# Kernel optimization log

Hardware: AMD Instinct MI355X
Metric: run time of the kernel (lower is better)

## Reference

```python
import jax, jax.numpy as jnp
import numpy as np
import math

NUM_HEADS = 8
LN_EPS = 1e-5
SINK_EPS = 1.0  # entropic eps in SinkhornDistance (eps=1)


def _layer_norm(x, g, b):
    m = jnp.mean(x, axis=-1, keepdims=True)
    v = jnp.var(x, axis=-1, keepdims=True)
    return (x - m) * jax.lax.rsqrt(v + LN_EPS) * g + b


def setup_inputs() -> dict:
    key = jax.random.key(0)
    ks = jax.random.split(key, 8)
    B, n, dQ, dV = 8, 1024, 512, 512
    s = 1.0 / math.sqrt(dV)
    return {
        "Q": jax.random.normal(ks[0], (B, n, dQ), jnp.float32),
        "K": jax.random.normal(ks[1], (B, n, dQ), jnp.float32),
        "Wq": jax.random.normal(ks[2], (dV, dQ), jnp.float32) * s,
        "bq": jax.random.normal(ks[3], (dV,), jnp.float32) * 0.01,
        "Wo": jax.random.normal(ks[4], (dV, dV), jnp.float32) * s,
        "bo": jax.random.normal(ks[5], (dV,), jnp.float32) * 0.01,
        "g0": jnp.ones((dV,), jnp.float32),
        "b0": jnp.zeros((dV,), jnp.float32),
        "g1": jnp.ones((dV,), jnp.float32),
        "b1": jnp.zeros((dV,), jnp.float32),
    }


def reference(Q, K, Wq, bq, Wo, bo, g0, b0, g1, b1):
    # K is accepted by the original forward but unused (K_ = V_ = Q_).
    B, n, _ = Q.shape
    dim_V = Wq.shape[0]
    H = NUM_HEADS
    d = dim_V // H

    Qp = Q @ Wq.T + bq                                   # [B, n, dim_V]
    # torch.cat(Q.split(d, 2), 0): head-major stacking -> [H*B, n, d]
    Q_ = Qp.reshape(B, n, H, d).transpose(2, 0, 1, 3).reshape(H * B, n, d)

    sqrtV = math.sqrt(math.sqrt(dim_V))
    X = Q_ / sqrtV
    # cost = dotmat(X, X) = -X X^T  (overall scaled by 1/sqrt(dim_V))
    C = -jnp.einsum('bnd,bmd->bnm', X, X)                # [HB, n, n]

    # log-domain Sinkhorn, eps=1, max_iter=1, mu = nu = 1/n
    log_mu = jnp.log(1.0 / n + 1e-8).astype(Q.dtype)
    M0 = -C / SINK_EPS
    u = SINK_EPS * (log_mu - jax.scipy.special.logsumexp(M0, axis=-1))         # [HB, n]
    v = SINK_EPS * (log_mu - jax.scipy.special.logsumexp(
        (-C + u[:, :, None]) / SINK_EPS, axis=1))                               # [HB, n]
    pi = jnp.exp((-C + u[:, :, None] + v[:, None, :]) / SINK_EPS)               # [HB, n, n]

    A = pi * n
    O_ = Q_ + jnp.einsum('bnm,bmd->bnd', A, Q_)          # [HB, n, d]
    # inverse head stacking -> [B, n, dim_V]
    O = O_.reshape(H, B, n, d).transpose(1, 2, 0, 3).reshape(B, n, dim_V)

    O = _layer_norm(O, g0, b0)
    O = O + jax.nn.relu(O @ Wo.T + bo)
    O = _layer_norm(O, g1, b1)
    return O
```

## Files before the change

kernel.cpp:

```cpp
#include <hip/hip_runtime.h>
#include <hip/hip_bf16.h>

typedef __bf16 bf16;
typedef __bf16 bf16x4 __attribute__((ext_vector_type(4)));
typedef __bf16 bf16x8 __attribute__((ext_vector_type(8)));
typedef float  f32x4  __attribute__((ext_vector_type(4)));

#define DEVI static __device__ __forceinline__

constexpr float SCALE_S = 0.04419417382415922f;
constexpr float LOG_MU  = -6.93146156565f;
constexpr int   LDT     = 72;

DEVI f32x4 mfma16(bf16x8 a, bf16x8 b, f32x4 c) {
    return __builtin_amdgcn_mfma_f32_16x16x32_bf16(a, b, c, 0, 0, 0);
}

DEVI bf16x8 cvt8(const float* __restrict__ p) {
    const float4 f0 = *(const float4*)p;
    const float4 f1 = *(const float4*)(p + 4);
    bf16x8 h;
    h[0] = (bf16)f0.x; h[1] = (bf16)f0.y; h[2] = (bf16)f0.z; h[3] = (bf16)f0.w;
    h[4] = (bf16)f1.x; h[5] = (bf16)f1.y; h[6] = (bf16)f1.z; h[7] = (bf16)f1.w;
    return h;
}

template<int EPI>
__global__ __launch_bounds__(256)
void gemm_kernel(const void* __restrict__ Ap, const float* __restrict__ Bm,
                 const float* __restrict__ bias, const bf16* __restrict__ X0,
                 bf16* __restrict__ outQh, bf16* __restrict__ outQhT,
                 float* __restrict__ outT)
{
    __shared__ bf16 sA[64 * LDT];
    __shared__ bf16 sB[64 * LDT];
    const int tid = threadIdx.x;
    const int rowBase = blockIdx.y * 64;
    const int colBase = blockIdx.x * 64;
    const int w = tid >> 6, lane = tid & 63, quad = lane >> 4, l16 = lane & 15;
    const int wr = (w >> 1) * 32, wc = (w & 1) * 32;

    f32x4 acc[2][2];
    #pragma unroll
    for (int i = 0; i < 2; ++i)
        #pragma unroll
        for (int j = 0; j < 2; ++j)
            #pragma unroll
            for (int e = 0; e < 4; ++e) acc[i][j][e] = 0.f;

    for (int kt = 0; kt < 512; kt += 64) {
        if (kt) __syncthreads();
        #pragma unroll
        for (int it = 0; it < 2; ++it) {
            int idx = it * 256 + tid;
            int r = idx >> 3, kb = idx & 7;
            if (EPI == 0) {
                *(bf16x8*)(&sA[r * LDT + kb * 8]) =
                    cvt8((const float*)Ap + (size_t)(rowBase + r) * 512 + kt + kb * 8);
            } else {
                *(uint4*)(&sA[r * LDT + kb * 8]) =
                    *(const uint4*)((const bf16*)Ap + (size_t)(rowBase + r) * 512 + kt + kb * 8);
            }
            *(bf16x8*)(&sB[r * LDT + kb * 8]) =
                cvt8(Bm + (size_t)(colBase + r) * 512 + kt + kb * 8);
        }
        __syncthreads();
        #pragma unroll
        for (int kk = 0; kk < 2; ++kk) {
            bf16x8 a[2], b[2];
            #pragma unroll
            for (int i = 0; i < 2; ++i)
                a[i] = *(const bf16x8*)(&sA[(wr + i * 16 + l16) * LDT + kk * 32 + quad * 8]);
            #pragma unroll
            for (int j = 0; j < 2; ++j)
                b[j] = *(const bf16x8*)(&sB[(wc + j * 16 + l16) * LDT + kk * 32 + quad * 8]);
            #pragma unroll
            for (int i = 0; i < 2; ++i)
                #pragma unroll
                for (int j = 0; j < 2; ++j)
                    acc[i][j] = mfma16(a[i], b[j], acc[i][j]);
        }
    }

    #pragma unroll
    for (int i = 0; i < 2; ++i) {
        #pragma unroll
        for (int j = 0; j < 2; ++j) {
            const int col = colBase + wc + j * 16 + l16;
            const float bv = bias[col];
            if (EPI == 0) {
                const int hh = col >> 6, jj = col & 63;
                const int rowA = rowBase + wr + i * 16 + quad * 4;
                const int bb = rowA >> 10, iib = rowA & 1023;
                const int bhh = (hh << 3) + bb;
                bf16x4 pk;
                #pragma unroll
                for (int rg = 0; rg < 4; ++rg) {
                    const float z = acc[i][j][rg] + bv;
                    pk[rg] = (bf16)z;
                    outQh[((size_t)(bhh * 1024 + iib + rg) << 6) + jj] = (bf16)z;
                }
                if (outQhT)
                    *(bf16x4*)(&outQhT[(((size_t)bhh * 64 + jj) << 10) + iib]) = pk;
            } else {
                #pragma unroll
                for (int rg = 0; rg < 4; ++rg) {
                    const int row = rowBase + wr + i * 16 + quad * 4 + rg;
                    const float z = acc[i][j][rg] + bv;
                    const float x0 = (float)X0[(size_t)row * 512 + col];
                    outT[(size_t)row * 512 + col] = x0 + fmaxf(z, 0.f);
                }
            }
        }
    }
}

template<int ADD_U>
__global__ __launch_bounds__(256, 4)
void sink_lse_kernel(const bf16* __restrict__ Qh, const float* __restrict__ uin,
                     float* __restrict__ out)
{
    __shared__ bf16 sQi[128 * LDT];
    __shared__ bf16 sQm[64 * LDT];
    __shared__ float su[1024];
    const int tid = threadIdx.x;
    const int bh = blockIdx.y;
    const int rowTile = blockIdx.x * 128;
    const bf16* Qb = Qh + ((size_t)bh << 16);

    #pragma unroll
    for (int it = 0; it < 4; ++it) {
        int idx = it * 256 + tid;
        int r = idx >> 3, kb = idx & 7;
        *(uint4*)(&sQi[r * LDT + kb * 8]) =
            *(const uint4*)(Qb + ((rowTile + r) << 6) + kb * 8);
    }
    if (ADD_U)
        *(float4*)(&su[tid * 4]) = *(const float4*)(uin + (bh << 10) + tid * 4);

    const int w = tid >> 6, lane = tid & 63, quad = lane >> 4, l16 = lane & 15;
    float rsum[2][4] = {{0.f,0.f,0.f,0.f},{0.f,0.f,0.f,0.f}};

    for (int mt = 0; mt < 16; ++mt) {
        __syncthreads();
        #pragma unroll
        for (int it = 0; it < 2; ++it) {
            int idx = it * 256 + tid;
            int r = idx >> 3, kb = idx & 7;
            *(uint4*)(&sQm[r * LDT + kb * 8]) =
                *(const uint4*)(Qb + ((mt * 64 + r) << 6) + kb * 8);
        }
        __syncthreads();

        f32x4 acc[2][4];
        #pragma unroll
        for (int a = 0; a < 2; ++a)
            #pragma unroll
            for (int ct = 0; ct < 4; ++ct)
                #pragma unroll
                for (int e = 0; e < 4; ++e) acc[a][ct][e] = 0.f;

        #pragma unroll
        for (int kk = 0; kk < 2; ++kk) {
            bf16x8 afr[2], bfr[4];
            #pragma unroll
            for (int a = 0; a < 2; ++a)
                afr[a] = *(const bf16x8*)(&sQi[(w * 32 + a * 16 + l16) * LDT + kk * 32 + quad * 8]);
            #pragma unroll
            for (int ct = 0; ct < 4; ++ct)
                bfr[ct] = *(const bf16x8*)(&sQm[(ct * 16 + l16) * LDT + kk * 32 + quad * 8]);
            #pragma unroll
            for (int a = 0; a < 2; ++a)
                #pragma unroll
                for (int ct = 0; ct < 4; ++ct)
                    acc[a][ct] = mfma16(afr[a], bfr[ct], acc[a][ct]);
        }
        #pragma unroll
        for (int a = 0; a < 2; ++a)
            #pragma unroll
            for (int ct = 0; ct < 4; ++ct) {
                const float uadd = ADD_U ? su[mt * 64 + ct * 16 + l16] : 0.f;
                #pragma unroll
                for (int rg = 0; rg < 4; ++rg)
                    rsum[a][rg] += __expf(acc[a][ct][rg] * SCALE_S + uadd);
            }
    }
    #pragma unroll
    for (int off = 1; off < 16; off <<= 1)
        #pragma unroll
        for (int a = 0; a < 2; ++a)
            #pragma unroll
            for (int rg = 0; rg < 4; ++rg)
                rsum[a][rg] += __shfl_xor(rsum[a][rg], off);

    if (l16 == 0) {
        #pragma unroll
        for (int a = 0; a < 2; ++a)
            #pragma unroll
            for (int rg = 0; rg < 4; ++rg)
                out[(bh << 10) + rowTile + w * 32 + a * 16 + quad * 4 + rg] =
                    LOG_MU - __logf(rsum[a][rg]);
    }
}

template<int USE_T>
__global__ __launch_bounds__(256, 2)
void sink_av_kernel(const bf16* __restrict__ Qh, const bf16* __restrict__ QhT,
                    const float* __restrict__ u, const float* __restrict__ v,
                    float* __restrict__ O)
{
    __shared__ bf16 sQi[128 * LDT];
    __shared__ bf16 sQm[64 * LDT];
    __shared__ bf16 sQmT[64 * LDT];
    __shared__ bf16 sP[4][32 * LDT];
    __shared__ float sv[1024];
    const int tid = threadIdx.x;
    const int bh = blockIdx.y;
    const int rowTile = blockIdx.x * 128;
    const bf16* Qb = Qh + ((size_t)bh << 16);
    const bf16* QbT = QhT + ((size_t)bh << 16);
    const int w = tid >> 6, lane = tid & 63, quad = lane >> 4, l16 = lane & 15;

    #pragma unroll
    for (int it = 0; it < 4; ++it) {
        int idx = it * 256 + tid;
        int r = idx >> 3, kb = idx & 7;
        *(uint4*)(&sQi[r * LDT + kb * 8]) =
            *(const uint4*)(Qb + ((rowTile + r) << 6) + kb * 8);
    }
    *(float4*)(&sv[tid * 4]) = *(const float4*)(v + (bh << 10) + tid * 4);
    float u_r[2][4];
    #pragma unroll
    for (int a = 0; a < 2; ++a)
        #pragma unroll
        for (int rg = 0; rg < 4; ++rg)
            u_r[a][rg] = u[(bh << 10) + rowTile + w * 32 + a * 16 + quad * 4 + rg];

    f32x4 accO[2][4];
    #pragma unroll
    for (int a = 0; a < 2; ++a)
        #pragma unroll
        for (int ct = 0; ct < 4; ++ct)
            #pragma unroll
            for (int e = 0; e < 4; ++e) accO[a][ct][e] = 0.f;

    for (int mt = 0; mt < 16; ++mt) {
        __syncthreads();
        #pragma unroll
        for (int it = 0; it < 2; ++it) {
            int idx = it * 256 + tid;
            int r = idx >> 3, kb = idx & 7;
            if (USE_T) {
                *(uint4*)(&sQm[r * LDT + kb * 8]) =
                    *(const uint4*)(Qb + ((mt * 64 + r) << 6) + kb * 8);
                *(uint4*)(&sQmT[r * LDT + kb * 8]) =
                    *(const uint4*)(QbT + (r << 10) + mt * 64 + kb * 8);
            } else {
                uint4 val = *(const uint4*)(Qb + ((mt * 64 + r) << 6) + kb * 8);
                *(uint4*)(&sQm[r * LDT + kb * 8]) = val;
                union { uint4 q; bf16 e[8]; } cv; cv.q = val;
                #pragma unroll
                for (int j = 0; j < 8; ++j)
                    sQmT[(kb * 8 + j) * LDT + r] = cv.e[j];
            }
        }
        __syncthreads();

        f32x4 acc[2][4];
        #pragma unroll
        for (int a = 0; a < 2; ++a)
            #pragma unroll
            for (int ct = 0; ct < 4; ++ct)
                #pragma unroll
                for (int e = 0; e < 4; ++e) acc[a][ct][e] = 0.f;

        #pragma unroll
        for (int kk = 0; kk < 2; ++kk) {
            bf16x8 afr[2], bfr[4];
            #pragma unroll
            for (int a = 0; a < 2; ++a)
                afr[a] = *(const bf16x8*)(&sQi[(w * 32 + a * 16 + l16) * LDT + kk * 32 + quad * 8]);
            #pragma unroll
            for (int ct = 0; ct < 4; ++ct)
                bfr[ct] = *(const bf16x8*)(&sQm[(ct * 16 + l16) * LDT + kk * 32 + quad * 8]);
            #pragma unroll
            for (int a = 0; a < 2; ++a)
                #pragma unroll
                for (int ct = 0; ct < 4; ++ct)
                    acc[a][ct] = mfma16(afr[a], bfr[ct], acc[a][ct]);
        }
        #pragma unroll
        for (int a = 0; a < 2; ++a)
            #pragma unroll
            for (int ct = 0; ct < 4; ++ct) {
                const float vv = sv[mt * 64 + ct * 16 + l16];
                #pragma unroll
                for (int rg = 0; rg < 4; ++rg) {
                    const float p = 1024.f * __expf(acc[a][ct][rg] * SCALE_S + u_r[a][rg] + vv);
                    sP[w][(a * 16 + quad * 4 + rg) * LDT + ct * 16 + l16] = (bf16)p;
                }
            }
        #pragma unroll
        for (int kk = 0; kk < 2; ++kk) {
            bf16x8 a2[2], b2[4];
            #pragma unroll
            for (int a = 0; a < 2; ++a)
                a2[a] = *(const bf16x8*)(&sP[w][(a * 16 + l16) * LDT + kk * 32 + quad * 8]);
            #pragma unroll
            for (int ct = 0; ct < 4; ++ct)
                b2[ct] = *(const bf16x8*)(&sQmT[(ct * 16 + l16) * LDT + kk * 32 + quad * 8]);
            #pragma unroll
            for (int a = 0; a < 2; ++a)
                #pragma unroll
                for (int ct = 0; ct < 4; ++ct)
                    accO[a][ct] = mfma16(a2[a], b2[ct], accO[a][ct]);
        }
    }

    const int hh = bh >> 3, bb = bh & 7;
    #pragma unroll
    for (int a = 0; a < 2; ++a)
        #pragma unroll
        for (int ct = 0; ct < 4; ++ct) {
            const int dcol = ct * 16 + l16;
            #pragma unroll
            for (int rg = 0; rg < 4; ++rg) {
                const int irow = w * 32 + a * 16 + quad * 4 + rg;
                const float o = (float)sQi[irow * LDT + dcol] + accO[a][ct][rg];
                O[((size_t)(bb * 1024 + rowTile + irow) << 9) + (hh << 6) + dcol] = o;
            }
        }
}

template<typename OutT>
__global__ __launch_bounds__(256)
void ln_kernel(const float* __restrict__ X, const float* __restrict__ g,
               const float* __restrict__ bb, OutT* __restrict__ out)
{
    const int row = blockIdx.x;
    const float* x = X + (size_t)row * 512;
    const float2 v2 = ((const float2*)x)[threadIdx.x];
    float s  = v2.x + v2.y;
    float ss = v2.x * v2.x + v2.y * v2.y;
    #pragma unroll
    for (int off = 32; off; off >>= 1) {
        s  += __shfl_down(s, off);
        ss += __shfl_down(ss, off);
    }
    __shared__ float red[8];
    const int w = threadIdx.x >> 6, lane = threadIdx.x & 63;
    if (lane == 0) { red[w] = s; red[4 + w] = ss; }
    __syncthreads();
    s  = red[0] + red[1] + red[2] + red[3];
    ss = red[4] + red[5] + red[6] + red[7];
    const float mean = s * (1.f / 512.f);
    const float var  = ss * (1.f / 512.f) - mean * mean;
    const float rstd = rsqrtf(var + 1e-5f);
    const int c = threadIdx.x * 2;
    const float y0 = (v2.x - mean) * rstd * g[c]     + bb[c];
    const float y1 = (v2.y - mean) * rstd * g[c + 1] + bb[c + 1];
    out[(size_t)row * 512 + c]     = (OutT)y0;
    out[(size_t)row * 512 + c + 1] = (OutT)y1;
}

extern "C" void kernel_launch(void* const* d_in, const int* in_sizes, int n_in,
                              void* d_out, int out_size, void* d_ws, size_t ws_size,
                              hipStream_t stream)
{
    const float* Q  = (const float*)d_in[0];
    const float* Wq = (const float*)d_in[2];
    const float* bq = (const float*)d_in[3];
    const float* Wo = (const float*)d_in[4];
    const float* bo = (const float*)d_in[5];
    const float* g0 = (const float*)d_in[6];
    const float* b0 = (const float*)d_in[7];
    const float* g1 = (const float*)d_in[8];
    const float* b1 = (const float*)d_in[9];

    char* ws = (char*)d_ws;
    const bool useT = ws_size >= (size_t)34078720;

    bf16 *Qh, *QhT, *X0;
    float *u, *v, *Obuf;
    if (useT) {
        Qh   = (bf16*)ws;
        QhT  = (bf16*)(ws + 8388608);
        X0   = (bf16*)(ws + 8388608);
        u    = (float*)(ws + 16777216);
        v    = (float*)(ws + 17039360);
        Obuf = (float*)(ws + 17301504);
    } else {
        Qh   = (bf16*)ws;
        QhT  = nullptr;
        X0   = (bf16*)ws;
        u    = (float*)(ws + 8388608);
        v    = (float*)(ws + 8650752);
        Obuf = (float*)(ws + 8912896);
    }

    gemm_kernel<0><<<dim3(8, 128), 256, 0, stream>>>(Q, Wq, bq, nullptr, Qh, QhT, nullptr);
    sink_lse_kernel<0><<<dim3(8, 64), 256, 0, stream>>>(Qh, nullptr, u);
    sink_lse_kernel<1><<<dim3(8, 64), 256, 0, stream>>>(Qh, u, v);
    if (useT)
        sink_av_kernel<1><<<dim3(8, 64), 256, 0, stream>>>(Qh, QhT, u, v, Obuf);
    else
        sink_av_kernel<0><<<dim3(8, 64), 256, 0, stream>>>(Qh, Qh, u, v, Obuf);
    ln_kernel<bf16><<<8192, 256, 0, stream>>>(Obuf, g0, b0, X0);
    gemm_kernel<1><<<dim3(8, 128), 256, 0, stream>>>(X0, Wo, bo, X0, nullptr, nullptr, Obuf);
    ln_kernel<float><<<8192, 256, 0, stream>>>(Obuf, g1, b1, (float*)d_out);
}
```

Baseline: 229.6 us.

## Double-buffer key tiles with register prefetch in Sinkhorn LSE and AV kernels

Both Sinkhorn kernels now prefetch the next 64-row key tile into registers at the start of each iteration and write it into a second shared-memory buffer after the compute. This overlaps global-load latency with the MFMA and exp work and cuts the two barriers per iteration down to one. In exchange it doubles the shared-memory footprint for the key tiles and raises register pressure, which may reduce occupancy, especially in the AV kernel that buffers both sQm and sQmT.

```diff
diff --git a/kernel.cpp b/kernel.cpp
--- a/kernel.cpp
+++ b/kernel.cpp
@@ -121,7 +121,7 @@
                      float* __restrict__ out)
 {
     __shared__ bf16 sQi[128 * LDT];
-    __shared__ bf16 sQm[64 * LDT];
+    __shared__ bf16 sQm[2][64 * LDT];
     __shared__ float su[1024];
     const int tid = threadIdx.x;
     const int bh = blockIdx.y;
@@ -138,19 +138,24 @@
     if (ADD_U)
         *(float4*)(&su[tid * 4]) = *(const float4*)(uin + (bh << 10) + tid * 4);
 
+    const int r0 = tid >> 3, kb0 = tid & 7;
+    #pragma unroll
+    for (int it = 0; it < 2; ++it)
+        *(uint4*)(&sQm[0][(it * 32 + r0) * LDT + kb0 * 8]) =
+            *(const uint4*)(Qb + ((it * 32 + r0) << 6) + kb0 * 8);
+    __syncthreads();
+
     const int w = tid >> 6, lane = tid & 63, quad = lane >> 4, l16 = lane & 15;
     float rsum[2][4] = {{0.f,0.f,0.f,0.f},{0.f,0.f,0.f,0.f}};
 
     for (int mt = 0; mt < 16; ++mt) {
-        __syncthreads();
-        #pragma unroll
-        for (int it = 0; it < 2; ++it) {
-            int idx = it * 256 + tid;
-            int r = idx >> 3, kb = idx & 7;
-            *(uint4*)(&sQm[r * LDT + kb * 8]) =
-                *(const uint4*)(Qb + ((mt * 64 + r) << 6) + kb * 8);
-        }
-        __syncthreads();
+        const int cur = mt & 1;
+        uint4 pf[2];
+        if (mt < 15) {
+            #pragma unroll
+            for (int it = 0; it < 2; ++it)
+                pf[it] = *(const uint4*)(Qb + (((mt + 1) * 64 + it * 32 + r0) << 6) + kb0 * 8);
+        }
 
         f32x4 acc[2][4];
         #pragma unroll
@@ -168,7 +173,7 @@
                 afr[a] = *(const bf16x8*)(&sQi[(w * 32 + a * 16 + l16) * LDT + kk * 32 + quad * 8]);
             #pragma unroll
             for (int ct = 0; ct < 4; ++ct)
-                bfr[ct] = *(const bf16x8*)(&sQm[(ct * 16 + l16) * LDT + kk * 32 + quad * 8]);
+                bfr[ct] = *(const bf16x8*)(&sQm[cur][(ct * 16 + l16) * LDT + kk * 32 + quad * 8]);
             #pragma unroll
             for (int a = 0; a < 2; ++a)
                 #pragma unroll
@@ -184,6 +189,13 @@
                 for (int rg = 0; rg < 4; ++rg)
                     rsum[a][rg] += __expf(acc[a][ct][rg] * SCALE_S + uadd);
             }
+
+        if (mt < 15) {
+            #pragma unroll
+            for (int it = 0; it < 2; ++it)
+                *(uint4*)(&sQm[cur ^ 1][(it * 32 + r0) * LDT + kb0 * 8]) = pf[it];
+        }
+        __syncthreads();
     }
     #pragma unroll
     for (int off = 1; off < 16; off <<= 1)
@@ -210,8 +222,8 @@
                     float* __restrict__ O)
 {
     __shared__ bf16 sQi[128 * LDT];
-    __shared__ bf16 sQm[64 * LDT];
-    __shared__ bf16 sQmT[64 * LDT];
+    __shared__ bf16 sQm[2][64 * LDT];
+    __shared__ bf16 sQmT[2][64 * LDT];
     __shared__ bf16 sP[4][32 * LDT];
     __shared__ float sv[1024];
     const int tid = threadIdx.x;
@@ -220,6 +232,7 @@
     const bf16* Qb = Qh + ((size_t)bh << 16);
     const bf16* QbT = QhT + ((size_t)bh << 16);
     const int w = tid >> 6, lane = tid & 63, quad = lane >> 4, l16 = lane & 15;
+    const int r0 = tid >> 3, kb0 = tid & 7;
 
     #pragma unroll
     for (int it = 0; it < 4; ++it) {
@@ -236,6 +249,23 @@
         for (int rg = 0; rg < 4; ++rg)
             u_r[a][rg] = u[(bh << 10) + rowTile + w * 32 + a * 16 + quad * 4 + rg];
 
+    #pragma unroll
+    for (int it = 0; it < 2; ++it) {
+        const int r = it * 32 + r0;
+        uint4 val = *(const uint4*)(Qb + (r << 6) + kb0 * 8);
+        *(uint4*)(&sQm[0][r * LDT + kb0 * 8]) = val;
+        if (USE_T) {
+            *(uint4*)(&sQmT[0][r * LDT + kb0 * 8]) =
+                *(const uint4*)(QbT + (r << 10) + kb0 * 8);
+        } else {
+            union { uint4 q; bf16 e[8]; } cv; cv.q = val;
+            #pragma unroll
+            for (int j = 0; j < 8; ++j)
+                sQmT[0][(kb0 * 8 + j) * LDT + r] = cv.e[j];
+        }
+    }
+    __syncthreads();
+
     f32x4 accO[2][4];
     #pragma unroll
     for (int a = 0; a < 2; ++a)
@@ -245,26 +275,17 @@
             for (int e = 0; e < 4; ++e) accO[a][ct][e] = 0.f;
 
     for (int mt = 0; mt < 16; ++mt) {
-        __syncthreads();
-        #pragma unroll
-        for (int it = 0; it < 2; ++it) {
-            int idx = it * 256 + tid;
-            int r = idx >> 3, kb = idx & 7;
-            if (USE_T) {
-                *(uint4*)(&sQm[r * LDT + kb * 8]) =
-                    *(const uint4*)(Qb + ((mt * 64 + r) << 6) + kb * 8);
-                *(uint4*)(&sQmT[r * LDT + kb * 8]) =
-                    *(const uint4*)(QbT + (r << 10) + mt * 64 + kb * 8);
-            } else {
-                uint4 val = *(const uint4*)(Qb + ((mt * 64 + r) << 6) + kb * 8);
-                *(uint4*)(&sQm[r * LDT + kb * 8]) = val;
-                union { uint4 q; bf16 e[8]; } cv; cv.q = val;
-                #pragma unroll
-                for (int j = 0; j < 8; ++j)
-                    sQmT[(kb * 8 + j) * LDT + r] = cv.e[j];
-            }
-        }
-        __syncthreads();
+        const int cur = mt & 1;
+        uint4 pfm[2], pft[2];
+        if (mt < 15) {
+            #pragma unroll
+            for (int it = 0; it < 2; ++it) {
+                const int r = it * 32 + r0;
+                pfm[it] = *(const uint4*)(Qb + (((mt + 1) * 64 + r) << 6) + kb0 * 8);
+                if (USE_T)
+                    pft[it] = *(const uint4*)(QbT + (r << 10) + (mt + 1) * 64 + kb0 * 8);
+            }
+        }
 
         f32x4 acc[2][4];
         #pragma unroll
@@ -282,7 +303,7 @@
                 afr[a] = *(const bf16x8*)(&sQi[(w * 32 + a * 16 + l16) * LDT + kk * 32 + quad * 8]);
             #pragma unroll
             for (int ct = 0; ct < 4; ++ct)
-                bfr[ct] = *(const bf16x8*)(&sQm[(ct * 16 + l16) * LDT + kk * 32 + quad * 8]);
+                bfr[ct] = *(const bf16x8*)(&sQm[cur][(ct * 16 + l16) * LDT + kk * 32 + quad * 8]);
             #pragma unroll
             for (int a = 0; a < 2; ++a)
                 #pragma unroll
@@ -308,13 +329,30 @@
                 a2[a] = *(const bf16x8*)(&sP[w][(a * 16 + l16) * LDT + kk * 32 + quad * 8]);
             #pragma unroll
             for (int ct = 0; ct < 4; ++ct)
-                b2[ct] = *(const bf16x8*)(&sQmT[(ct * 16 + l16) * LDT + kk * 32 + quad * 8]);
+                b2[ct] = *(const bf16x8*)(&sQmT[cur][(ct * 16 + l16) * LDT + kk * 32 + quad * 8]);
             #pragma unroll
             for (int a = 0; a < 2; ++a)
                 #pragma unroll
                 for (int ct = 0; ct < 4; ++ct)
                     accO[a][ct] = mfma16(a2[a], b2[ct], accO[a][ct]);
         }
+
+        if (mt < 15) {
+            #pragma unroll
+            for (int it = 0; it < 2; ++it) {
+                const int r = it * 32 + r0;
+                *(uint4*)(&sQm[cur ^ 1][r * LDT + kb0 * 8]) = pfm[it];
+                if (USE_T) {
+                    *(uint4*)(&sQmT[cur ^ 1][r * LDT + kb0 * 8]) = pft[it];
+                } else {
+                    union { uint4 q; bf16 e[8]; } cv; cv.q = pfm[it];
+                    #pragma unroll
+                    for (int j = 0; j < 8; ++j)
+                        sQmT[cur ^ 1][(kb0 * 8 + j) * LDT + r] = cv.e[j];
+                }
+            }
+        }
+        __syncthreads();
     }
 
     const int hh = bh >> 3, bb = bh & 7;
```

Measured after the change: 228.3 us. About the same (-0.6%).
